# Kernel optimization log

Hardware: AMD Instinct MI355X
Metric: run time of the kernel (lower is better)

Reference implementation:

```python
import jax, jax.numpy as jnp
import numpy as np

# Four fixed 3x3 'gradient' kernels (left, right, up, down), stacked as OIHW (4,1,3,3).
_K = np.zeros((4, 1, 3, 3), np.float32)
_K[0, 0, 1, 0] = -1.0; _K[0, 0, 1, 1] = 1.0   # left:  center - left neighbor
_K[1, 0, 1, 1] = 1.0;  _K[1, 0, 1, 2] = -1.0  # right: center - right neighbor
_K[2, 0, 0, 1] = -1.0; _K[2, 0, 1, 1] = 1.0   # up:    center - upper neighbor
_K[3, 0, 1, 1] = 1.0;  _K[3, 0, 2, 1] = -1.0  # down:  center - lower neighbor
KERNELS = jnp.asarray(_K)

LOSS_WEIGHT = 1.0
POOL = 4


def _avgpool4(x):
    # AvgPool2d(4) on NCHW with H,W divisible by 4
    b, c, h, w = x.shape
    return x.reshape(b, c, h // POOL, POOL, w // POOL, POOL).mean(axis=(3, 5))


def _grad_conv(x):
    # F.conv2d(x, kernels, padding=1); x: (B,1,Hp,Wp) -> (B,4,Hp,Wp)
    return jax.lax.conv_general_dilated(
        x, KERNELS, window_strides=(1, 1), padding=((1, 1), (1, 1)),
        dimension_numbers=('NCHW', 'OIHW', 'NCHW'))


def setup_inputs() -> dict:
    key = jax.random.key(0)
    k1, k2 = jax.random.split(key)
    B, C, H, W = 32, 3, 512, 512
    x = jax.random.uniform(k1, (B, C, H, W), dtype=jnp.float32)
    pred = jax.random.uniform(k2, (B, C, H, W), dtype=jnp.float32)
    return {"x": x, "pred": pred}


def reference(x, pred):
    # channel mean -> (B,1,H,W), then 4x4 average pool -> (B,1,H/4,W/4)
    org_pool = _avgpool4(jnp.mean(x, axis=1, keepdims=True))
    enh_pool = _avgpool4(jnp.mean(pred, axis=1, keepdims=True))
    # NOTE: the original computes weight_diff and E_1 but never uses them in the
    # returned loss, so they are omitted (no effect on output or gradients).
    d = _grad_conv(org_pool) - _grad_conv(enh_pool)  # (B,4,Hp,Wp)
    # mean(D_left + D_right + D_up + D_down) == mean over (B,Hp,Wp) of channel-sum
    E = jnp.mean(jnp.sum(d * d, axis=1))
    return LOSS_WEIGHT * E
```

## Files before the change

kernel.cpp:

```cpp
#include <hip/hip_runtime.h>

constexpr int B  = 32;
constexpr int C  = 3;
constexpr int H  = 512;
constexpr int W  = 512;
constexpr int HP = H / 4;
constexpr int WP = W / 4;
constexpr int NP = B * HP * WP;
constexpr int W4 = W / 4;

constexpr int ROWS_PB     = 8;
constexpr int HROWS       = ROWS_PB + 1;
constexpr int BLK_PER_IMG = HP / ROWS_PB;
constexpr int NBLOCKS     = B * BLK_PER_IMG;
constexpr int NTASK       = C * HROWS * WP;

__global__ __launch_bounds__(1024, 8) void spatial_loss_fused(
        const float* __restrict__ x,
        const float* __restrict__ pred,
        float* __restrict__ out) {
    __shared__ float sm[C * HROWS][WP];
    __shared__ float P[HROWS][WP];
    __shared__ float ws_red[16];

    int orig = blockIdx.x;
    int blk  = (orig & 7) * (NBLOCKS / 8) + (orig >> 3);
    int b    = blk >> 4;
    int br   = blk & 15;
    int py0  = br * ROWS_PB;
    int tid  = threadIdx.x;

    const float4* __restrict__ xb = (const float4*)x;
    const float4* __restrict__ pb = (const float4*)pred;

    for (int t = tid; t < NTASK; t += 1024) {
        int q  = t & 127;
        int cr = t >> 7;
        int rr = cr / 3;
        int c  = cr - 3 * rr;
        int gy = py0 + rr - 1;
        float s = 0.0f;
        if (gy >= 0) {
            int a = ((b * C + c) * H + gy * 4) * W4 + q;
            float4 x0 = xb[a];
            float4 x1 = xb[a + W4];
            float4 x2 = xb[a + 2 * W4];
            float4 x3 = xb[a + 3 * W4];
            float4 p0 = pb[a];
            float4 p1 = pb[a + W4];
            float4 p2 = pb[a + 2 * W4];
            float4 p3 = pb[a + 3 * W4];
            float s0 = (x0.x - p0.x) + (x0.y - p0.y) + (x0.z - p0.z) + (x0.w - p0.w);
            float s1 = (x1.x - p1.x) + (x1.y - p1.y) + (x1.z - p1.z) + (x1.w - p1.w);
            float s2 = (x2.x - p2.x) + (x2.y - p2.y) + (x2.z - p2.z) + (x2.w - p2.w);
            float s3 = (x3.x - p3.x) + (x3.y - p3.y) + (x3.z - p3.z) + (x3.w - p3.w);
            s = (s0 + s1) + (s2 + s3);
        }
        sm[cr][q] = s;
    }
    __syncthreads();

    for (int i = tid; i < HROWS * WP; i += 1024) {
        int q  = i & 127;
        int pr = i >> 7;
        P[pr][q] = (sm[3 * pr][q] + sm[3 * pr + 1][q] + sm[3 * pr + 2][q])
                   * (1.0f / 48.0f);
    }
    __syncthreads();

    float acc;
    {
        int q  = tid & 127;
        int r  = tid >> 7;
        int gy = py0 + r;
        float cv = P[r + 1][q];
        float up = P[r][q];
        float lf = (q > 0) ? P[r + 1][q - 1] : 0.0f;
        float dy = cv - up;
        float dx = cv - lf;
        float wy = (gy > 0) ? 2.0f : 1.0f;
        float wx = (q  > 0) ? 2.0f : 1.0f;
        acc = wy * dy * dy + wx * dx * dx;
        if (gy == HP - 1) acc += cv * cv;
        if (q  == WP - 1) acc += cv * cv;
    }

    #pragma unroll
    for (int off = 32; off > 0; off >>= 1)
        acc += __shfl_down(acc, off, 64);

    int lane = tid & 63;
    int wid  = tid >> 6;
    if (lane == 0) ws_red[wid] = acc;
    __syncthreads();
    if (tid == 0) {
        float s = 0.0f;
        #pragma unroll
        for (int k = 0; k < 16; ++k) s += ws_red[k];
        atomicAdd(out, s * (1.0f / (float)NP));
    }
}

extern "C" void kernel_launch(void* const* d_in, const int* in_sizes, int n_in,
                              void* d_out, int out_size, void* d_ws, size_t ws_size,
                              hipStream_t stream) {
    const float* x    = (const float*)d_in[0];
    const float* pred = (const float*)d_in[1];
    float* out = (float*)d_out;

    hipMemsetAsync(out, 0, sizeof(float), stream);

    spatial_loss_fused<<<NBLOCKS, 1024, 0, stream>>>(x, pred, out);
}
```

Before: 221.7 us.

## Double rows per block to cut halo reloads and use nontemporal loads

Each block now covers 16 pooled rows instead of 8, halving the block count. This cuts the fraction of redundant halo-row reads from global memory, and each thread accumulates two output positions. Input loads switch to nontemporal builtins so the streamed data does not pollute the caches. The trade-off is fewer blocks (256 of 1024 threads) for the 256 CUs, lower occupancy, and a larger shared-memory footprint.

```diff
diff --git a/kernel.cpp b/kernel.cpp
--- a/kernel.cpp
+++ b/kernel.cpp
@@ -9,13 +9,16 @@
 constexpr int NP = B * HP * WP;
 constexpr int W4 = W / 4;
 
-constexpr int ROWS_PB     = 8;
+typedef float f4 __attribute__((ext_vector_type(4)));
+
+constexpr int ROWS_PB     = 16;
 constexpr int HROWS       = ROWS_PB + 1;
 constexpr int BLK_PER_IMG = HP / ROWS_PB;
 constexpr int NBLOCKS     = B * BLK_PER_IMG;
+constexpr int NTHR        = 1024;
 constexpr int NTASK       = C * HROWS * WP;
 
-__global__ __launch_bounds__(1024, 8) void spatial_loss_fused(
+__global__ __launch_bounds__(1024, 1) void spatial_loss_fused(
         const float* __restrict__ x,
         const float* __restrict__ pred,
         float* __restrict__ out) {
@@ -25,15 +28,15 @@
 
     int orig = blockIdx.x;
     int blk  = (orig & 7) * (NBLOCKS / 8) + (orig >> 3);
-    int b    = blk >> 4;
-    int br   = blk & 15;
+    int b    = blk >> 3;
+    int br   = blk & 7;
     int py0  = br * ROWS_PB;
     int tid  = threadIdx.x;
 
-    const float4* __restrict__ xb = (const float4*)x;
-    const float4* __restrict__ pb = (const float4*)pred;
+    const f4* __restrict__ xb = (const f4*)x;
+    const f4* __restrict__ pb = (const f4*)pred;
 
-    for (int t = tid; t < NTASK; t += 1024) {
+    for (int t = tid; t < NTASK; t += NTHR) {
         int q  = t & 127;
         int cr = t >> 7;
         int rr = cr / 3;
@@ -42,14 +45,14 @@
         float s = 0.0f;
         if (gy >= 0) {
             int a = ((b * C + c) * H + gy * 4) * W4 + q;
-            float4 x0 = xb[a];
-            float4 x1 = xb[a + W4];
-            float4 x2 = xb[a + 2 * W4];
-            float4 x3 = xb[a + 3 * W4];
-            float4 p0 = pb[a];
-            float4 p1 = pb[a + W4];
-            float4 p2 = pb[a + 2 * W4];
-            float4 p3 = pb[a + 3 * W4];
+            f4 x0 = __builtin_nontemporal_load(xb + a);
+            f4 x1 = __builtin_nontemporal_load(xb + a + W4);
+            f4 x2 = __builtin_nontemporal_load(xb + a + 2 * W4);
+            f4 x3 = __builtin_nontemporal_load(xb + a + 3 * W4);
+            f4 p0 = __builtin_nontemporal_load(pb + a);
+            f4 p1 = __builtin_nontemporal_load(pb + a + W4);
+            f4 p2 = __builtin_nontemporal_load(pb + a + 2 * W4);
+            f4 p3 = __builtin_nontemporal_load(pb + a + 3 * W4);
             float s0 = (x0.x - p0.x) + (x0.y - p0.y) + (x0.z - p0.z) + (x0.w - p0.w);
             float s1 = (x1.x - p1.x) + (x1.y - p1.y) + (x1.z - p1.z) + (x1.w - p1.w);
             float s2 = (x2.x - p2.x) + (x2.y - p2.y) + (x2.z - p2.z) + (x2.w - p2.w);
@@ -60,7 +63,7 @@
     }
     __syncthreads();
 
-    for (int i = tid; i < HROWS * WP; i += 1024) {
+    for (int i = tid; i < HROWS * WP; i += NTHR) {
         int q  = i & 127;
         int pr = i >> 7;
         P[pr][q] = (sm[3 * pr][q] + sm[3 * pr + 1][q] + sm[3 * pr + 2][q])
@@ -68,10 +71,12 @@
     }
     __syncthreads();
 
-    float acc;
-    {
-        int q  = tid & 127;
-        int r  = tid >> 7;
+    float acc = 0.0f;
+    #pragma unroll
+    for (int j = 0; j < (ROWS_PB * WP) / NTHR; ++j) {
+        int i  = tid + j * NTHR;
+        int q  = i & 127;
+        int r  = i >> 7;
         int gy = py0 + r;
         float cv = P[r + 1][q];
         float up = P[r][q];
@@ -80,7 +85,7 @@
         float dx = cv - lf;
         float wy = (gy > 0) ? 2.0f : 1.0f;
         float wx = (q  > 0) ? 2.0f : 1.0f;
-        acc = wy * dy * dy + wx * dx * dx;
+        acc += wy * dy * dy + wx * dx * dx;
         if (gy == HP - 1) acc += cv * cv;
         if (q  == WP - 1) acc += cv * cv;
     }
@@ -110,5 +115,5 @@
 
     hipMemsetAsync(out, 0, sizeof(float), stream);
 
-    spatial_loss_fused<<<NBLOCKS, 1024, 0, stream>>>(x, pred, out);
+    spatial_loss_fused<<<NBLOCKS, NTHR, 0, stream>>>(x, pred, out);
 }
```

Result: faster. 194.4 us, median of 2 (-12.3%).
